# Kernel optimization log

Measured on AMD Instinct MI355X. Metric: run time of the kernel, lower is better.

## Reference

```python
import jax, jax.numpy as jnp
import numpy as np

HID, H, HD, K, L = 512, 8, 64, 64, 767  # hidden, heads, head_dim, clip, coord length
B, S = 2, L + 1  # add_cls pads one token


def _rel_indices(coords, k):
    # torch.cdist p=2: pairwise euclidean distances [B, L, L]
    diff = coords[:, :, None, :] - coords[:, None, :, :]
    dist = jnp.sqrt(jnp.sum(diff * diff, axis=-1))
    # rank along rows / columns via double argsort
    t1 = jnp.argsort(jnp.argsort(dist, axis=-1), axis=-1)
    t2 = jnp.argsort(jnp.argsort(dist, axis=-2), axis=-2)
    nm = jnp.triu(t1, k=1) + jnp.tril(t2, k=1)
    nm = jnp.clip(nm, 0, k)
    # add_cls: prepend a zero column then a zero row -> [B, L+1, L+1]
    nm = jnp.pad(nm, ((0, 0), (1, 0), (1, 0)))
    return nm.astype(jnp.int32)


def setup_inputs() -> dict:
    key = jax.random.key(0)
    ks = jax.random.split(key, 16)
    sc = 0.05
    return {
        "query": jax.random.normal(ks[0], (B, S, HID), jnp.float32),
        "key": jax.random.normal(ks[1], (B, S, HID), jnp.float32),
        "value": jax.random.normal(ks[2], (B, S, HID), jnp.float32),
        "coords": jax.random.normal(ks[3], (B, L, 2), jnp.float32),
        "Wq": jax.random.normal(ks[4], (H, HID, HD), jnp.float32) * sc,
        "bq": jax.random.normal(ks[5], (H, HD), jnp.float32) * sc,
        "Wk": jax.random.normal(ks[6], (H, HID, HD), jnp.float32) * sc,
        "bk": jax.random.normal(ks[7], (H, HD), jnp.float32) * sc,
        "Wv": jax.random.normal(ks[8], (H, HID, HD), jnp.float32) * sc,
        "bv": jax.random.normal(ks[9], (H, HD), jnp.float32) * sc,
        "pe_k": jax.random.normal(ks[10], (K + 1, HD), jnp.float32) * sc,
        "pe_v": jax.random.normal(ks[11], (K + 1, HD), jnp.float32) * sc,
        "fc_W": jax.random.normal(ks[12], (HID, HID), jnp.float32) * sc,
        "fc_b": jax.random.normal(ks[13], (HID,), jnp.float32) * sc,
    }


def reference(query, key, value, coords, Wq, bq, Wk, bk, Wv, bv, pe_k, pe_v, fc_W, fc_b):
    idx = _rel_indices(coords, K)                 # [B, S, S] int
    k_bias = pe_k[idx]                            # [B, S, S, HD]
    v_bias = pe_v[idx]                            # [B, S, S, HD]

    # per-head projections, heads stacked on axis n
    q = jnp.einsum('bsh,nhd->bnsd', query, Wq) + bq[None, :, None, :]
    k = jnp.einsum('bsh,nhd->bnsd', key, Wk) + bk[None, :, None, :]
    v = jnp.einsum('bsh,nhd->bnsd', value, Wv) + bv[None, :, None, :]

    attn1 = jnp.einsum('bnqd,bnkd->bnqk', q, k)
    attn2 = jnp.einsum('bnqd,bqkd->bnqk', q, k_bias)  # per-query relative key bias
    att = jax.nn.softmax((attn1 + attn2) / (HD ** 0.5), axis=-1)

    out1 = jnp.einsum('bnqk,bnkd->bnqd', att, v)
    out2 = jnp.einsum('bnqk,bqkd->bnqd', att, v_bias)  # relative value bias
    heads = (out1 + out2).transpose(0, 2, 1, 3).reshape(B, S, H * HD)  # concat heads
    return heads @ fc_W.T + fc_b
```

## Files before the change

### kernel.cpp

```cpp
#include <hip/hip_runtime.h>
#include <math.h>

#define HIDD 512
#define NH 8
#define HD 64
#define KCLIP 64
#define LCO 767
#define BB 2
#define SS 768

#define TQ 32
#define KT 64
#define NT (SS / KT)
#define KS 4
#define TPB (NT / KS)
#define NROW (BB * NH * SS)
#define QPAD 68

__global__ __launch_bounds__(256) void rel_idx_kernel(
    const float* __restrict__ coords, int* __restrict__ idx)
{
    __shared__ float cx[LCO], cy[LCO];
    __shared__ unsigned long long dk[LCO];
    const int blk = blockIdx.x;
    const int b = blk / LCO;
    const int i = blk % LCO;
    const int t = threadIdx.x;
    const float* cb = coords + (size_t)b * LCO * 2;
    for (int j = t; j < LCO; j += 256) {
        float2 c2 = *(const float2*)(cb + 2 * j);
        cx[j] = c2.x; cy[j] = c2.y;
    }
    __syncthreads();
    const float xi = cx[i], yi = cy[i];
    for (int j = t; j < LCO; j += 256) {
        float dx = xi - cx[j];
        float dy = yi - cy[j];
        float d2 = __fadd_rn(__fmul_rn(dx, dx), __fmul_rn(dy, dy));
        float d = sqrtf(d2);
        dk[j] = ((unsigned long long)__float_as_uint(d) << 32) | (unsigned)j;
    }
    __syncthreads();
    if (i + 1 + t >= LCO) return;

    unsigned long long myk[3] = {0ull, 0ull, 0ull};
    int js[3] = {0, 0, 0};
    int cnt[3] = {0, 0, 0};
    int nreal = 0;
    for (int j = i + 1 + t; j < LCO; j += 256) {
        js[nreal] = j; myk[nreal] = dk[j]; ++nreal;
    }
    for (int jp = 0; jp < LCO; ++jp) {
        unsigned long long kv = dk[jp];
        cnt[0] += (kv < myk[0]);
        cnt[1] += (kv < myk[1]);
        cnt[2] += (kv < myk[2]);
    }
    int* ib = idx + (size_t)b * SS * SS;
    for (int u = 0; u < nreal; ++u) {
        int r = cnt[u] > KCLIP ? KCLIP : cnt[u];
        int j = js[u];
        ib[(i + 1) * SS + (j + 1)] = r;
        ib[(j + 1) * SS + (i + 1)] = r;
    }
}

__global__ __launch_bounds__(256) void proj_kernel(
    const float* __restrict__ qin, const float* __restrict__ kin, const float* __restrict__ vin,
    const float* __restrict__ Wq, const float* __restrict__ Wk, const float* __restrict__ Wv,
    const float* __restrict__ bq, const float* __restrict__ bk, const float* __restrict__ bv,
    float* __restrict__ qo, float* __restrict__ kTo, float* __restrict__ vo)
{
    const int z = blockIdx.z;
    const float* A = (z == 0) ? qin : (z == 1) ? kin : vin;
    const float* W = (z == 0) ? Wq : (z == 1) ? Wk : Wv;
    const float* bias = (z == 0) ? bq : (z == 1) ? bk : bv;
    const int h = blockIdx.y;
    const int m0 = blockIdx.x * 64;

    __shared__ float As[32][68];
    __shared__ float Bs[32][64];

    const int t = threadIdx.x;
    const int tx = t & 15, ty = t >> 4;
    const float* Wh = W + (size_t)h * HIDD * HD;

    float acc[4][4] = {};
    for (int k0 = 0; k0 < HIDD; k0 += 32) {
#pragma unroll
        for (int u = 0; u < 2; ++u) {
            int i = t + u * 256;
            int row = i >> 3, kc = (i & 7) * 4;
            float4 a4 = *(const float4*)(A + (size_t)(m0 + row) * HIDD + k0 + kc);
            As[kc + 0][row] = a4.x; As[kc + 1][row] = a4.y;
            As[kc + 2][row] = a4.z; As[kc + 3][row] = a4.w;
            int kr = i >> 4, n4 = (i & 15) * 4;
            *(float4*)(&Bs[kr][n4]) = *(const float4*)(Wh + (size_t)(k0 + kr) * HD + n4);
        }
        __syncthreads();
#pragma unroll
        for (int kk = 0; kk < 32; ++kk) {
            float4 a4 = *(const float4*)(&As[kk][ty * 4]);
            float4 b4 = *(const float4*)(&Bs[kk][tx * 4]);
            float a_[4] = {a4.x, a4.y, a4.z, a4.w};
            float b_[4] = {b4.x, b4.y, b4.z, b4.w};
#pragma unroll
            for (int r = 0; r < 4; ++r)
#pragma unroll
                for (int c = 0; c < 4; ++c) acc[r][c] += a_[r] * b_[c];
        }
        __syncthreads();
    }
#pragma unroll
    for (int r = 0; r < 4; ++r) {
        int m = m0 + ty * 4 + r;
        int bIdx = m / SS, s = m % SS;
#pragma unroll
        for (int c = 0; c < 4; ++c) {
            int d = tx * 4 + c;
            float val = acc[r][c] + bias[h * HD + d];
            if (z == 1) {
                kTo[((size_t)(bIdx * NH + h) * HD + d) * SS + s] = val;
            } else {
                float* O = (z == 0) ? qo : vo;
                O[((size_t)(bIdx * NH + h) * SS + s) * HD + d] = val;
            }
        }
    }
}

__global__ __launch_bounds__(256) void qpk_kernel(
    const float* __restrict__ q, const float* __restrict__ pe_k, float* __restrict__ qpkg)
{
    __shared__ float qs[64][68];
    __shared__ float pk[65][68];
    const int t = threadIdx.x;
    const int q0 = blockIdx.x * 64;
    const int bn = blockIdx.y;
    const float* qbase = q + ((size_t)bn * SS + q0) * HD;
    for (int i = t; i < 64 * 16; i += 256) {
        int row = i >> 4, d4 = (i & 15) * 4;
        *(float4*)(&qs[row][d4]) = *(const float4*)(qbase + (size_t)row * HD + d4);
    }
    for (int i = t; i < 65 * 16; i += 256) {
        int c = i >> 4, d4 = (i & 15) * 4;
        *(float4*)(&pk[c][d4]) = *(const float4*)(pe_k + (size_t)c * HD + d4);
    }
    __syncthreads();
    const int r0 = t >> 2, cg = t & 3;
    float* orow = qpkg + ((size_t)bn * SS + q0 + r0) * QPAD;
    for (int c = cg; c <= KCLIP; c += 4) {
        float acc = 0.f;
#pragma unroll
        for (int d4 = 0; d4 < HD; d4 += 4) {
            float4 qv = *(const float4*)(&qs[r0][d4]);
            float4 pv = *(const float4*)(&pk[c][d4]);
            acc += qv.x * pv.x + qv.y * pv.y + qv.z * pv.z + qv.w * pv.w;
        }
        orow[c] = acc;
    }
}

__global__ __launch_bounds__(256) void attn_part_kernel(
    const float* __restrict__ q, const float* __restrict__ kT,
    const float* __restrict__ vb, const int* __restrict__ idx,
    const float* __restrict__ qpkg,
    float* __restrict__ o1p, float* __restrict__ pspart, float* __restrict__ wbpart)
{
    __shared__ float qsT[HD][TQ];
    __shared__ float kv[KT][HD];
    __shared__ float attQ[TQ][68];
    __shared__ float qpkS[TQ][68];
    __shared__ float wbuf[TQ][KCLIP];

    const int t = threadIdx.x;
    const int bn = blockIdx.y;
    const int b = bn >> 3;
    const int q0 = blockIdx.x * TQ;
    const int ks = blockIdx.z;

    const int qh = t >> 4;
    const int kg = t & 15;

    const float* qbase = q + ((size_t)bn * SS + q0) * HD;
    for (int i = t; i < TQ * 16; i += 256) {
        int r = i >> 4, dx = (i & 15) * 4;
        float4 v4 = *(const float4*)(qbase + (size_t)r * HD + dx);
        qsT[dx + 0][r] = v4.x; qsT[dx + 1][r] = v4.y;
        qsT[dx + 2][r] = v4.z; qsT[dx + 3][r] = v4.w;
    }
    for (int i = t; i < TQ * 17; i += 256) {
        int r = i / 17, c4 = (i % 17) * 4;
        *(float4*)(&qpkS[r][c4]) = *(const float4*)(qpkg + ((size_t)bn * SS + q0 + r) * QPAD + c4);
    }
    for (int i = t; i < TQ * KCLIP; i += 256) ((float*)wbuf)[i] = 0.f;
    __syncthreads();

    const float* kTbn = kT + (size_t)bn * HD * SS;
    const float* vbn = vb + (size_t)bn * SS * HD;
    const int* ib = idx + (size_t)b * SS * SS;

    float out1[2][4] = {};
    float psum[2] = {0.f, 0.f};

    for (int t0 = 0; t0 < TPB; ++t0) {
        const int k0 = (ks * TPB + t0) * KT;
        for (int i = t; i < KT * 16; i += 256) {
            int d = i >> 4, c4 = (i & 15) * 4;
            *(float4*)(&kv[d][c4]) = *(const float4*)(kTbn + (size_t)d * SS + k0 + c4);
        }
        __syncthreads();

        float acc[2][4] = {};
#pragma unroll 16
        for (int d = 0; d < HD; ++d) {
            float q0v = qsT[d][2 * qh];
            float q1v = qsT[d][2 * qh + 1];
            float4 k4 = *(const float4*)(&kv[d][4 * kg]);
            acc[0][0] += q0v * k4.x; acc[0][1] += q0v * k4.y;
            acc[0][2] += q0v * k4.z; acc[0][3] += q0v * k4.w;
            acc[1][0] += q1v * k4.x; acc[1][1] += q1v * k4.y;
            acc[1][2] += q1v * k4.z; acc[1][3] += q1v * k4.w;
        }
#pragma unroll
        for (int e = 0; e < 2; ++e) {
            int qq = 2 * qh + e;
            int4 iv = *(const int4*)(ib + (size_t)(q0 + qq) * SS + k0 + 4 * kg);
            float p0 = expf((acc[e][0] + qpkS[qq][iv.x]) * 0.125f);
            float p1 = expf((acc[e][1] + qpkS[qq][iv.y]) * 0.125f);
            float p2 = expf((acc[e][2] + qpkS[qq][iv.z]) * 0.125f);
            float p3 = expf((acc[e][3] + qpkS[qq][iv.w]) * 0.125f);
            float4 pv4; pv4.x = p0; pv4.y = p1; pv4.z = p2; pv4.w = p3;
            *(float4*)(&attQ[qq][4 * kg]) = pv4;
            if (iv.x < KCLIP) atomicAdd(&wbuf[qq][iv.x], p0);
            if (iv.y < KCLIP) atomicAdd(&wbuf[qq][iv.y], p1);
            if (iv.z < KCLIP) atomicAdd(&wbuf[qq][iv.z], p2);
            if (iv.w < KCLIP) atomicAdd(&wbuf[qq][iv.w], p3);
            psum[e] += p0 + p1 + p2 + p3;
        }
        __syncthreads();

        for (int i = t; i < KT * 16; i += 256) {
            int k = i >> 4, d4 = (i & 15) * 4;
            *(float4*)(&kv[k][d4]) = *(const float4*)(vbn + (size_t)(k0 + k) * HD + d4);
        }
        __syncthreads();

#pragma unroll 16
        for (int k = 0; k < KT; ++k) {
            float a0 = attQ[2 * qh][k];
            float a1 = attQ[2 * qh + 1][k];
            float4 v4 = *(const float4*)(&kv[k][4 * kg]);
            out1[0][0] += a0 * v4.x; out1[0][1] += a0 * v4.y;
            out1[0][2] += a0 * v4.z; out1[0][3] += a0 * v4.w;
            out1[1][0] += a1 * v4.x; out1[1][1] += a1 * v4.y;
            out1[1][2] += a1 * v4.z; out1[1][3] += a1 * v4.w;
        }
        __syncthreads();
    }

#pragma unroll
    for (int off = 8; off; off >>= 1) {
        psum[0] += __shfl_xor(psum[0], off);
        psum[1] += __shfl_xor(psum[1], off);
    }
    const size_t rbase = (size_t)ks * NROW + (size_t)bn * SS + q0;
    if (kg == 0) {
        pspart[rbase + 2 * qh] = psum[0];
        pspart[rbase + 2 * qh + 1] = psum[1];
    }
#pragma unroll
    for (int e = 0; e < 2; ++e) {
        int qq = 2 * qh + e;
        *(float4*)(o1p + (rbase + qq) * HD + 4 * kg) = *(float4*)(out1[e]);
    }
    for (int i = t; i < TQ * KCLIP / 4; i += 256) {
        int r = i >> 4, c4 = (i & 15) * 4;
        *(float4*)(wbpart + (rbase + r) * KCLIP + c4) = *(const float4*)(&wbuf[r][c4]);
    }
}

__global__ __launch_bounds__(256) void attn_combine_kernel(
    const float* __restrict__ o1p, const float* __restrict__ pspart,
    const float* __restrict__ wbpart, const float* __restrict__ pe_v,
    float* __restrict__ heads)
{
    __shared__ float wl[4][66];
    const int t = threadIdx.x;
    const int rt = t >> 6, d = t & 63;
    const int row = blockIdx.x * 4 + rt;
    const int bn = row / SS, qq = row % SS;
    const int b = bn >> 3, n = bn & 7;

    float w = 0.f, rsum = 0.f, o = 0.f;
#pragma unroll
    for (int ks = 0; ks < KS; ++ks) {
        w += wbpart[((size_t)ks * NROW + row) * KCLIP + d];
        rsum += pspart[(size_t)ks * NROW + row];
        o += o1p[((size_t)ks * NROW + row) * HD + d];
    }
    wl[rt][d] = w;
    __syncthreads();

    const float pv64 = pe_v[KCLIP * HD + d];
    float acc = o;
#pragma unroll 8
    for (int c = 0; c < KCLIP; ++c)
        acc += wl[rt][c] * (pe_v[c * HD + d] - pv64);
    heads[((size_t)b * SS + qq) * HIDD + n * HD + d] = acc / rsum + pv64;
}

__global__ __launch_bounds__(256) void fc_kernel(
    const float* __restrict__ heads, const float* __restrict__ fcW,
    const float* __restrict__ fcb, float* __restrict__ out)
{
    const int m0 = blockIdx.x * 32;
    const int n0 = blockIdx.y * 64;

    __shared__ float As[32][36];
    __shared__ float Bs[32][64];

    const int t = threadIdx.x;
    const int ty = t >> 4;
    const int tx = t & 15;

    float acc[2][4] = {};
    for (int k0 = 0; k0 < HIDD; k0 += 32) {
        {
            int row = t >> 3, kc = (t & 7) * 4;
            float4 a4 = *(const float4*)(heads + (size_t)(m0 + row) * HIDD + k0 + kc);
            As[kc + 0][row] = a4.x; As[kc + 1][row] = a4.y;
            As[kc + 2][row] = a4.z; As[kc + 3][row] = a4.w;
        }
#pragma unroll
        for (int u = 0; u < 2; ++u) {
            int i = t + u * 256;
            int nl = i >> 3, kl = (i & 7) * 4;
            float4 bw = *(const float4*)(fcW + (size_t)(n0 + nl) * HIDD + k0 + kl);
            Bs[kl + 0][nl] = bw.x; Bs[kl + 1][nl] = bw.y;
            Bs[kl + 2][nl] = bw.z; Bs[kl + 3][nl] = bw.w;
        }
        __syncthreads();
#pragma unroll
        for (int kk = 0; kk < 32; ++kk) {
            float a0 = As[kk][2 * ty];
            float a1 = As[kk][2 * ty + 1];
            float4 b4 = *(const float4*)(&Bs[kk][4 * tx]);
            acc[0][0] += a0 * b4.x; acc[0][1] += a0 * b4.y;
            acc[0][2] += a0 * b4.z; acc[0][3] += a0 * b4.w;
            acc[1][0] += a1 * b4.x; acc[1][1] += a1 * b4.y;
            acc[1][2] += a1 * b4.z; acc[1][3] += a1 * b4.w;
        }
        __syncthreads();
    }
    float4 bb = *(const float4*)(fcb + n0 + 4 * tx);
#pragma unroll
    for (int e = 0; e < 2; ++e) {
        float4 r4;
        r4.x = acc[e][0] + bb.x; r4.y = acc[e][1] + bb.y;
        r4.z = acc[e][2] + bb.z; r4.w = acc[e][3] + bb.w;
        *(float4*)(out + (size_t)(m0 + 2 * ty + e) * HIDD + n0 + 4 * tx) = r4;
    }
}

extern "C" void kernel_launch(void* const* d_in, const int* in_sizes, int n_in,
                              void* d_out, int out_size, void* d_ws, size_t ws_size,
                              hipStream_t stream)
{
    (void)in_sizes; (void)n_in; (void)out_size; (void)ws_size;
    const float* query  = (const float*)d_in[0];
    const float* key_   = (const float*)d_in[1];
    const float* value  = (const float*)d_in[2];
    const float* coords = (const float*)d_in[3];
    const float* Wq = (const float*)d_in[4];
    const float* bq = (const float*)d_in[5];
    const float* Wk = (const float*)d_in[6];
    const float* bk = (const float*)d_in[7];
    const float* Wv = (const float*)d_in[8];
    const float* bv = (const float*)d_in[9];
    const float* pe_k = (const float*)d_in[10];
    const float* pe_v = (const float*)d_in[11];
    const float* fcW  = (const float*)d_in[12];
    const float* fcb  = (const float*)d_in[13];
    float* out = (float*)d_out;

    char* ws = (char*)d_ws;
    size_t off = 0;
    auto alloc = [&](size_t bytes) -> void* {
        void* p = ws + off;
        off += (bytes + 255) & ~(size_t)255;
        return p;
    };
    int*   idx    = (int*)  alloc((size_t)BB * SS * SS * sizeof(int));
    float* qb     = (float*)alloc((size_t)BB * NH * SS * HD * sizeof(float));
    float* kTb    = (float*)alloc((size_t)BB * NH * HD * SS * sizeof(float));
    float* vb     = (float*)alloc((size_t)BB * NH * SS * HD * sizeof(float));
    float* headb  = (float*)alloc((size_t)BB * SS * HIDD * sizeof(float));
    float* qpkg   = (float*)alloc((size_t)NROW * QPAD * sizeof(float));
    float* o1p    = (float*)alloc((size_t)KS * NROW * HD * sizeof(float));
    float* pspart = (float*)alloc((size_t)KS * NROW * sizeof(float));
    float* wbpart = (float*)alloc((size_t)KS * NROW * KCLIP * sizeof(float));

    hipMemsetAsync(idx, 0, (size_t)BB * SS * SS * sizeof(int), stream);

    rel_idx_kernel<<<BB * LCO, 256, 0, stream>>>(coords, idx);

    proj_kernel<<<dim3((BB * SS) / 64, NH, 3), 256, 0, stream>>>(
        query, key_, value, Wq, Wk, Wv, bq, bk, bv, qb, kTb, vb);

    qpk_kernel<<<dim3(SS / 64, BB * NH), 256, 0, stream>>>(qb, pe_k, qpkg);

    attn_part_kernel<<<dim3(SS / TQ, BB * NH, KS), 256, 0, stream>>>(
        qb, kTb, vb, idx, qpkg, o1p, pspart, wbpart);

    attn_combine_kernel<<<NROW / 4, 256, 0, stream>>>(o1p, pspart, wbpart, pe_v, headb);

    fc_kernel<<<dim3((BB * SS) / 32, HIDD / 64), 256, 0, stream>>>(headb, fcW, fcb, out);
}
```

Measured before the change: 303.7 us.

## Rank neighbors via distance histogram threshold instead of all-pairs counting

The rank computation in rel_idx_kernel no longer compares every element against all others. It builds a shared-memory histogram of distances, finds the bucket where the cumulative count reaches the clip value, compacts only those candidates with a ballot, and ranks them among themselves. All other entries are set to the clip value by a new fill kernel that replaces the memset and also zeroes the padding row, padding column and diagonal. This removes the O(L^2) comparison work per row, at the cost of extra synchronisation and atomics, and the candidate count depends on how the distances are spread.

```diff
diff --git a/kernel.cpp b/kernel.cpp
--- a/kernel.cpp
+++ b/kernel.cpp
@@ -17,16 +17,41 @@
 #define NROW (BB * NH * SS)
 #define QPAD 68
 
+__global__ __launch_bounds__(256) void idx_fill_kernel(int* __restrict__ idx)
+{
+    size_t gid = (size_t)blockIdx.x * 256 + threadIdx.x;
+    size_t base = gid * 4;
+    int rem = (int)(base % (size_t)(SS * SS));
+    int r = rem / SS, c0 = rem % SS;
+    int4 v;
+    int* vv = (int*)&v;
+#pragma unroll
+    for (int u = 0; u < 4; ++u) {
+        int c = c0 + u;
+        vv[u] = (r == 0 || c == 0 || r == c) ? 0 : KCLIP;
+    }
+    *(int4*)(idx + base) = v;
+}
+
 __global__ __launch_bounds__(256) void rel_idx_kernel(
     const float* __restrict__ coords, int* __restrict__ idx)
 {
     __shared__ float cx[LCO], cy[LCO];
     __shared__ unsigned long long dk[LCO];
+    __shared__ unsigned long long lst[LCO];
+    __shared__ int hist[256];
+    __shared__ int cum[256];
+    __shared__ int nsel;
+    __shared__ int thrB;
+
     const int blk = blockIdx.x;
     const int b = blk / LCO;
     const int i = blk % LCO;
     const int t = threadIdx.x;
     const float* cb = coords + (size_t)b * LCO * 2;
+
+    hist[t] = 0;
+    if (t == 0) nsel = 0;
     for (int j = t; j < LCO; j += 256) {
         float2 c2 = *(const float2*)(cb + 2 * j);
         cx[j] = c2.x; cy[j] = c2.y;
@@ -39,29 +64,59 @@
         float d2 = __fadd_rn(__fmul_rn(dx, dx), __fmul_rn(dy, dy));
         float d = sqrtf(d2);
         dk[j] = ((unsigned long long)__float_as_uint(d) << 32) | (unsigned)j;
-    }
-    __syncthreads();
-    if (i + 1 + t >= LCO) return;
-
-    unsigned long long myk[3] = {0ull, 0ull, 0ull};
-    int js[3] = {0, 0, 0};
-    int cnt[3] = {0, 0, 0};
-    int nreal = 0;
-    for (int j = i + 1 + t; j < LCO; j += 256) {
-        js[nreal] = j; myk[nreal] = dk[j]; ++nreal;
-    }
-    for (int jp = 0; jp < LCO; ++jp) {
-        unsigned long long kv = dk[jp];
-        cnt[0] += (kv < myk[0]);
-        cnt[1] += (kv < myk[1]);
-        cnt[2] += (kv < myk[2]);
-    }
+        int bkt = (int)(d * 32.0f);
+        bkt = bkt > 255 ? 255 : bkt;
+        atomicAdd(&hist[bkt], 1);
+    }
+    __syncthreads();
+
+    cum[t] = hist[t];
+    __syncthreads();
+    for (int off = 1; off < 256; off <<= 1) {
+        int add = (t >= off) ? cum[t - off] : 0;
+        __syncthreads();
+        cum[t] += add;
+        __syncthreads();
+    }
+    if (cum[t] >= KCLIP && (t == 0 || cum[t - 1] < KCLIP)) thrB = t;
+    __syncthreads();
+    const int B = thrB;
+
+    const int lane = t & 63;
+#pragma unroll
+    for (int u = 0; u < 3; ++u) {
+        int j = t + u * 256;
+        bool sel = false;
+        unsigned long long key = 0;
+        if (j < LCO) {
+            key = dk[j];
+            float d = __uint_as_float((unsigned)(key >> 32));
+            int bkt = (int)(d * 32.0f);
+            bkt = bkt > 255 ? 255 : bkt;
+            sel = (bkt <= B);
+        }
+        unsigned long long m = __ballot(sel);
+        int base;
+        if (lane == 0) base = atomicAdd(&nsel, __popcll(m));
+        base = __shfl(base, 0);
+        if (sel) {
+            int pfx = __popcll(m & ((1ull << lane) - 1));
+            lst[base + pfx] = key;
+        }
+    }
+    __syncthreads();
+    const int C = nsel;
+
     int* ib = idx + (size_t)b * SS * SS;
-    for (int u = 0; u < nreal; ++u) {
-        int r = cnt[u] > KCLIP ? KCLIP : cnt[u];
-        int j = js[u];
-        ib[(i + 1) * SS + (j + 1)] = r;
-        ib[(j + 1) * SS + (i + 1)] = r;
+    for (int c = t; c < C; c += 256) {
+        unsigned long long myk = lst[c];
+        int cnt = 0;
+        for (int c2 = 0; c2 < C; ++c2) cnt += (lst[c2] < myk);
+        int j = (int)(myk & 0xffffffffu);
+        if (cnt < KCLIP && j > i) {
+            ib[(size_t)(i + 1) * SS + (j + 1)] = cnt;
+            ib[(size_t)(j + 1) * SS + (i + 1)] = cnt;
+        }
     }
 }
 
@@ -401,7 +456,7 @@
     float* pspart = (float*)alloc((size_t)KS * NROW * sizeof(float));
     float* wbpart = (float*)alloc((size_t)KS * NROW * KCLIP * sizeof(float));
 
-    hipMemsetAsync(idx, 0, (size_t)BB * SS * SS * sizeof(int), stream);
+    idx_fill_kernel<<<(BB * SS * SS) / (256 * 4), 256, 0, stream>>>(idx);
 
     rel_idx_kernel<<<BB * LCO, 256, 0, stream>>>(coords, idx);
 
```

New measurement: 247.2 us. 18.6% less time.
